# Optimization experiments

Hardware: AMD Instinct MI355X
Metric: run time of the kernel (lower is better)

The kernel has to match this reference:

```python
import jax, jax.numpy as jnp
import numpy as np

B, N, E, A, H, NT, TE = 2, 20000, 20000, 8, 256, 16, 32


def layer_norm(x, g, b, eps=1e-5):
    mu = x.mean(-1, keepdims=True)
    var = ((x - mu) ** 2).mean(-1, keepdims=True)
    return (x - mu) * jax.lax.rsqrt(var + eps) * g + b


def setup_inputs() -> dict:
    key = jax.random.key(0)
    ks = jax.random.split(key, 12)
    node_features = jax.random.normal(ks[0], (B, N, H), jnp.float32)
    hyperedge_members = jax.random.randint(ks[1], (B, E, A), 0, N)
    hyperedge_types = jax.random.randint(ks[2], (B, E), 0, NT)
    hyperedge_mask = jax.random.bernoulli(ks[3], 0.8, (B, E, A))
    edge_type_table = jax.random.normal(ks[4], (NT, TE), jnp.float32)
    W_enc = jax.random.normal(ks[5], (H + TE, H), jnp.float32) / np.sqrt(H + TE)
    b_enc = jnp.zeros((H,), jnp.float32)
    g_enc = jnp.ones((H,), jnp.float32)
    be_enc = jnp.zeros((H,), jnp.float32)
    W_upd = jax.random.normal(ks[6], (2 * H, H), jnp.float32) / np.sqrt(2 * H)
    b_upd = jnp.zeros((H,), jnp.float32)
    g_upd = jnp.ones((H,), jnp.float32)
    be_upd = jnp.zeros((H,), jnp.float32)
    return dict(node_features=node_features, hyperedge_members=hyperedge_members,
                hyperedge_types=hyperedge_types, hyperedge_mask=hyperedge_mask,
                edge_type_table=edge_type_table, W_enc=W_enc, b_enc=b_enc,
                g_enc=g_enc, be_enc=be_enc, W_upd=W_upd, b_upd=b_upd,
                g_upd=g_upd, be_upd=be_upd)


def reference(node_features, hyperedge_members, hyperedge_types, hyperedge_mask,
              edge_type_table, W_enc, b_enc, g_enc, be_enc,
              W_upd, b_upd, g_upd, be_upd):
    b, n, h = node_features.shape
    members = jnp.clip(hyperedge_members, 0, n - 1)          # [B,E,A]
    m = hyperedge_mask.astype(node_features.dtype)           # [B,E,A]

    # gather member features per hyperedge: [B,E,A,H]
    gathered = jax.vmap(lambda nf, idx: nf[idx])(node_features, members)
    gathered = gathered * m[..., None]
    cnt = jnp.clip(m.sum(-1, keepdims=True), 1.0, None)       # [B,E,1]
    pooled = gathered.sum(2) / cnt                            # [B,E,H]

    edge_emb = edge_type_table[hyperedge_types]               # [B,E,32]
    x = jnp.concatenate([pooled, edge_emb], -1) @ W_enc + b_enc
    edge_feat = layer_norm(jax.nn.gelu(x, approximate=False), g_enc, be_enc)  # [B,E,H]

    # scatter-add edge features back to member nodes (masked)
    def scat(ef, idx, mm):
        contrib = (ef[:, None, :] * mm[..., None]).reshape(-1, h)   # [E*A,H]
        flat = idx.reshape(-1)
        upd = jnp.zeros((n, h), ef.dtype).at[flat].add(contrib)
        c = jnp.zeros((n,), ef.dtype).at[flat].add(mm.reshape(-1))
        return upd, c

    upd, c = jax.vmap(scat)(edge_feat, members, m)            # [B,N,H], [B,N]
    upd = upd / jnp.clip(c, 1.0, None)[..., None]

    y = jnp.concatenate([node_features, upd], -1) @ W_upd + b_upd
    return layer_norm(jax.nn.gelu(y, approximate=False), g_upd, be_upd)
```

## Files before the change

kernel.cpp:

```cpp
#include <hip/hip_runtime.h>
#include <math.h>

#define Bq 2
#define Nn 20000
#define Ee 20000
#define Aa 8
#define Hh 256
#define TEe 32
#define NTy 16
constexpr int BE   = Bq * Ee;
constexpr int BN   = Bq * Nn;
constexpr int KTE  = 8;
constexpr int KTU  = 16;
constexpr int LDA  = 264;
constexpr int CAP  = 64;
constexpr int PB_DET = 256;
constexpr int PB_ZD  = 64;
constexpr int NINIT  = PB_DET + PB_ZD + 1;
constexpr int PB_PKE  = 32;
constexpr int PB_PKU  = 64;
constexpr int PB_TB   = 1;
constexpr int PB_FILL = 640;
constexpr int NPREP   = PB_PKE + PB_PKU + PB_TB + PB_FILL;

typedef __attribute__((ext_vector_type(8))) short bf16x8;
typedef __attribute__((ext_vector_type(4))) float f32x4;
typedef unsigned short u16;
typedef unsigned int   u32;

__device__ __forceinline__ u16 f2bf(float f) {
    u32 u = __float_as_uint(f);
    u32 r = u + 0x7FFFu + ((u >> 16) & 1u);
    return (u16)(r >> 16);
}
__device__ __forceinline__ float bf2f(u16 h) {
    return __uint_as_float(((u32)h) << 16);
}
__device__ __forceinline__ float gelu_f(float x) {
    return 0.5f * x * (1.f + erff(x * 0.70710678118654752440f));
}
__device__ __forceinline__ f32x4 mfma16(bf16x8 a, bf16x8 b, f32x4 c) {
    return __builtin_amdgcn_mfma_f32_16x16x32_bf16(a, b, c, 0, 0, 0);
}

__device__ __forceinline__ float mask_at(const void* mp, int flag, int i) {
    if (flag & 2) return ((const float*)mp)[i];
    if (flag & 1) return ((const unsigned char*)mp)[i] ? 1.f : 0.f;
    return ((const int*)mp)[i] ? 1.f : 0.f;
}

__global__ __launch_bounds__(256) void k_init(const unsigned int* __restrict__ mw,
                                              int nmw, int* __restrict__ flag,
                                              int* __restrict__ deg,
                                              float4* __restrict__ dummy) {
    const int bid = blockIdx.x;
    const int tid = threadIdx.x;
    if (bid < PB_DET) {
        int found = 0;
        for (int i = bid * 256 + tid; i < nmw; i += PB_DET * 256) {
            unsigned int w = mw[i];
            if (w == 0x3F800000u) found |= 2;
            else if (w > 1u) found |= 1;
        }
        __shared__ int sf;
        if (tid == 0) sf = 0;
        __syncthreads();
        if (found) atomicOr(&sf, found);
        __syncthreads();
        if (tid == 0 && sf) atomicOr(flag, sf);
    } else if (bid < PB_DET + PB_ZD) {
        for (int i = (bid - PB_DET) * 256 + tid; i < BN; i += PB_ZD * 256)
            deg[i] = 0;
    } else {
        if (tid < Hh * 2 / 16) {
            float4 z; z.x = 0.f; z.y = 0.f; z.z = 0.f; z.w = 0.f;
            dummy[tid] = z;
        }
    }
}

__global__ __launch_bounds__(256) void k_prep(
    const float* __restrict__ Wenc, u16* __restrict__ WeP,
    const float* __restrict__ Wupd, u16* __restrict__ WuP,
    const float* __restrict__ ett, const float* __restrict__ benc,
    float* __restrict__ tb,
    const int* __restrict__ members, const void* __restrict__ maskp,
    const int* __restrict__ flagp, int* __restrict__ deg,
    int* __restrict__ list2) {
    __shared__ float s_e[NTy * TEe];
    const int bid = blockIdx.x;
    const int tid = threadIdx.x;

    if (bid < PB_PKE) {
        int t = bid * 256 + tid;
        int lane = t & 63, tile = t >> 6;
        int kt = tile % KTE, nt = tile / KTE;
        int kbase = kt * 32 + (lane >> 4) * 8;
        int col = nt * 16 + (lane & 15);
        u16 tmp[8];
        #pragma unroll
        for (int j = 0; j < 8; j++)
            tmp[j] = f2bf(Wenc[(size_t)(kbase + j) * Hh + col]);
        *(uint4*)(WeP + (size_t)t * 8) = *(const uint4*)tmp;
    } else if (bid < PB_PKE + PB_PKU) {
        int t = (bid - PB_PKE) * 256 + tid;
        int lane = t & 63, tile = t >> 6;
        int kt = tile % KTU, nt = tile / KTU;
        int kbase = kt * 32 + (lane >> 4) * 8;
        int col = nt * 16 + (lane & 15);
        u16 tmp[8];
        #pragma unroll
        for (int j = 0; j < 8; j++)
            tmp[j] = f2bf(Wupd[(size_t)(kbase + j) * Hh + col]);
        *(uint4*)(WuP + (size_t)t * 8) = *(const uint4*)tmp;
    } else if (bid < PB_PKE + PB_PKU + PB_TB) {
        for (int i = tid; i < NTy * TEe; i += 256) s_e[i] = ett[i];
        __syncthreads();
        float b = benc[tid];
        for (int t = 0; t < NTy; t++) {
            float acc = b;
            #pragma unroll 8
            for (int k = 0; k < TEe; k++)
                acc = fmaf(s_e[t * TEe + k], Wenc[(size_t)(Hh + k) * Hh + tid], acc);
            tb[t * Hh + tid] = acc;
        }
    } else {
        int flag = flagp[0];
        int cbid = bid - (PB_PKE + PB_PKU + PB_TB);
        for (int i = cbid * 256 + tid; i < BE * Aa; i += PB_FILL * 256) {
            if (mask_at(maskp, flag, i) != 0.f) {
                int ge = i >> 3;
                int b = ge / Ee;
                int idx = min(max(members[i], 0), Nn - 1);
                int node = b * Nn + idx;
                int slot = atomicAdd(&deg[node], 1);
                if (slot < CAP) list2[(size_t)node * CAP + slot] = ge;
            }
        }
    }
}

__global__ __launch_bounds__(256) void k_dualgemm(
    const float* __restrict__ nf, const bf16x8* __restrict__ WeP,
    const bf16x8* __restrict__ WuP, uint4* __restrict__ nfWe1,
    uint4* __restrict__ nfW1) {
    __shared__ __align__(16) u16 s_a[32][LDA];
    const int tid = threadIdx.x;
    const int n0  = blockIdx.x * 32;
    const int w = tid >> 6, lane = tid & 63;
    const int l15 = lane & 15, lg = lane >> 4;

    {
        const float4* nf4 = (const float4*)nf + (size_t)n0 * 64;
        #pragma unroll
        for (int i = 0; i < 8; i++) {
            int idx = i * 256 + tid;
            int r = idx >> 6, cc = idx & 63;
            float4 v = nf4[r * 64 + cc];
            ushort4 u; u.x = f2bf(v.x); u.y = f2bf(v.y);
            u.z = f2bf(v.z); u.w = f2bf(v.w);
            *(ushort4*)&s_a[r][cc * 4] = u;
        }
    }
    __syncthreads();

    f32x4 accE[2][4], accU[2][4];
    #pragma unroll
    for (int m = 0; m < 2; m++)
        #pragma unroll
        for (int n = 0; n < 4; n++) {
            accE[m][n] = (f32x4){0.f, 0.f, 0.f, 0.f};
            accU[m][n] = (f32x4){0.f, 0.f, 0.f, 0.f};
        }

    #pragma unroll
    for (int kt = 0; kt < 8; kt++) {
        bf16x8 afr[2], bfrE[4], bfrU[4];
        #pragma unroll
        for (int n = 0; n < 4; n++) {
            bfrE[n] = WeP[((size_t)((w * 4 + n) * KTE + kt)) * 64 + lane];
            bfrU[n] = WuP[((size_t)((w * 4 + n) * KTU + kt)) * 64 + lane];
        }
        #pragma unroll
        for (int m = 0; m < 2; m++)
            afr[m] = *(const bf16x8*)&s_a[m * 16 + l15][kt * 32 + lg * 8];
        #pragma unroll
        for (int m = 0; m < 2; m++)
            #pragma unroll
            for (int n = 0; n < 4; n++) {
                accE[m][n] = mfma16(afr[m], bfrE[n], accE[m][n]);
                accU[m][n] = mfma16(afr[m], bfrU[n], accU[m][n]);
            }
    }
    __syncthreads();
    #pragma unroll
    for (int m = 0; m < 2; m++)
        #pragma unroll
        for (int j = 0; j < 4; j++) {
            int r = m * 16 + lg * 4 + j;
            #pragma unroll
            for (int n = 0; n < 4; n++)
                s_a[r][w * 64 + n * 16 + l15] = f2bf(accE[m][n][j]);
        }
    __syncthreads();
    {
        const uint4* sa4 = (const uint4*)&s_a[0][0];
        #pragma unroll
        for (int i = 0; i < 4; i++) {
            int idx = i * 256 + tid;
            int r = idx >> 5, cc = idx & 31;
            nfWe1[(size_t)(n0 + r) * 32 + cc] = sa4[r * 33 + cc];
        }
    }
    __syncthreads();
    #pragma unroll
    for (int m = 0; m < 2; m++)
        #pragma unroll
        for (int j = 0; j < 4; j++) {
            int r = m * 16 + lg * 4 + j;
            #pragma unroll
            for (int n = 0; n < 4; n++)
                s_a[r][w * 64 + n * 16 + l15] = f2bf(accU[m][n][j]);
        }
    __syncthreads();
    {
        const uint4* sa4 = (const uint4*)&s_a[0][0];
        #pragma unroll
        for (int i = 0; i < 4; i++) {
            int idx = i * 256 + tid;
            int r = idx >> 5, cc = idx & 31;
            nfW1[(size_t)(n0 + r) * 32 + cc] = sa4[r * 33 + cc];
        }
    }
}

__global__ __launch_bounds__(256) void k_edge_w2(
    const int* __restrict__ members, const void* __restrict__ maskp,
    const int* __restrict__ flagp, const int* __restrict__ types,
    const u16* __restrict__ nfWe1, const float* __restrict__ tb,
    const float* __restrict__ genc, const float* __restrict__ beenc,
    const bf16x8* __restrict__ WuP, uint4* __restrict__ efW2) {
    __shared__ __align__(16) u16 s_a[32][LDA];
    const int tid = threadIdx.x;
    const int e0  = blockIdx.x * 32;
    const int w = tid >> 6, lane = tid & 63;
    const int l15 = lane & 15, lg = lane >> 4;
    const int flag = flagp[0];
    const int c4 = lane * 4;

    {
        const int ew0 = e0 + w * 8;
        int base = ew0 * Aa + lane;
        int mem_all = members[base];
        float mv_all = mask_at(maskp, flag, base);
        int er = ew0 + (lane >> 3);
        int idxv = min(max(mem_all, 0), Nn - 1) + ((er >= Ee) ? Nn : 0);

        float4 gm = *(const float4*)(genc + c4);
        float4 bt = *(const float4*)(beenc + c4);

        for (int i = 0; i < 8; i++) {
            int e = ew0 + i;
            int idx[Aa]; float m[Aa];
            float c = 0.f;
            #pragma unroll
            for (int a = 0; a < Aa; a++) {
                idx[a] = __shfl(idxv, i * Aa + a, 64);
                m[a]   = __shfl(mv_all, i * Aa + a, 64);
                c += m[a];
            }
            const float rc = 1.f / fmaxf(c, 1.f);
            ushort4 v[Aa];
            #pragma unroll
            for (int a = 0; a < Aa; a++)
                v[a] = *(const ushort4*)(nfWe1 + (size_t)idx[a] * Hh + c4);
            float a0 = 0.f, a1 = 0.f, a2 = 0.f, a3 = 0.f;
            #pragma unroll
            for (int a = 0; a < Aa; a++) {
                a0 = fmaf(m[a], bf2f(v[a].x), a0);
                a1 = fmaf(m[a], bf2f(v[a].y), a1);
                a2 = fmaf(m[a], bf2f(v[a].z), a2);
                a3 = fmaf(m[a], bf2f(v[a].w), a3);
            }
            int t = types[e];
            float4 tbv = *(const float4*)(tb + t * Hh + c4);
            float g0 = gelu_f(fmaf(a0, rc, tbv.x));
            float g1 = gelu_f(fmaf(a1, rc, tbv.y));
            float g2 = gelu_f(fmaf(a2, rc, tbv.z));
            float g3 = gelu_f(fmaf(a3, rc, tbv.w));

            float s  = g0 + g1 + g2 + g3;
            float s2 = fmaf(g0, g0, fmaf(g1, g1, fmaf(g2, g2, g3 * g3)));
            #pragma unroll
            for (int mk = 1; mk < 64; mk <<= 1) {
                s  += __shfl_xor(s, mk, 64);
                s2 += __shfl_xor(s2, mk, 64);
            }
            float mu = s * (1.f / Hh);
            float rs = rsqrtf(s2 * (1.f / Hh) - mu * mu + 1e-5f);
            ushort4 o;
            o.x = f2bf((g0 - mu) * rs * gm.x + bt.x);
            o.y = f2bf((g1 - mu) * rs * gm.y + bt.y);
            o.z = f2bf((g2 - mu) * rs * gm.z + bt.z);
            o.w = f2bf((g3 - mu) * rs * gm.w + bt.w);
            *(ushort4*)&s_a[w * 8 + i][c4] = o;
        }
    }
    __syncthreads();

    f32x4 acc[2][4];
    #pragma unroll
    for (int m = 0; m < 2; m++)
        #pragma unroll
        for (int n = 0; n < 4; n++) acc[m][n] = (f32x4){0.f, 0.f, 0.f, 0.f};

    #pragma unroll
    for (int kt = 0; kt < 8; kt++) {
        bf16x8 bfr[4], afr[2];
        #pragma unroll
        for (int n = 0; n < 4; n++)
            bfr[n] = WuP[((size_t)((w * 4 + n) * KTU + 8 + kt)) * 64 + lane];
        #pragma unroll
        for (int m = 0; m < 2; m++)
            afr[m] = *(const bf16x8*)&s_a[m * 16 + l15][kt * 32 + lg * 8];
        #pragma unroll
        for (int m = 0; m < 2; m++)
            #pragma unroll
            for (int n = 0; n < 4; n++)
                acc[m][n] = mfma16(afr[m], bfr[n], acc[m][n]);
    }
    __syncthreads();
    #pragma unroll
    for (int m = 0; m < 2; m++)
        #pragma unroll
        for (int j = 0; j < 4; j++) {
            int r = m * 16 + lg * 4 + j;
            #pragma unroll
            for (int n = 0; n < 4; n++)
                s_a[r][w * 64 + n * 16 + l15] = f2bf(acc[m][n][j]);
        }
    __syncthreads();
    const uint4* sa4 = (const uint4*)&s_a[0][0];
    #pragma unroll
    for (int i = 0; i < 4; i++) {
        int idx = i * 256 + tid;
        int r = idx >> 5, cc = idx & 31;
        efW2[(size_t)(e0 + r) * 32 + cc] = sa4[r * 33 + cc];
    }
}

__global__ __launch_bounds__(512) void k_node_final(
    const u16* __restrict__ efW2, const u16* __restrict__ nfW1,
    const int* __restrict__ deg, const int* __restrict__ list2,
    const float* __restrict__ bupd, const float* __restrict__ gupd,
    const float* __restrict__ beupd, float* __restrict__ out) {
    const int n = (blockIdx.x * 512 + threadIdx.x) >> 6;
    const int lane = threadIdx.x & 63;
    if (n >= BN) return;
    const int d = min(deg[n], CAP);
    const size_t base = (size_t)n * CAP;
    const int c4 = lane * 4;

    float a0 = 0.f, a1 = 0.f, a2 = 0.f, a3 = 0.f;
    for (int j0 = 0; j0 < d; j0 += 8) {
        int lv = (lane < 8 && (j0 + lane) < d) ? list2[base + j0 + lane] : BE;
        ushort4 v[8];
        #pragma unroll
        for (int q = 0; q < 8; q++) {
            int ge = __shfl(lv, q, 64);
            v[q] = *(const ushort4*)(efW2 + (size_t)ge * Hh + c4);
        }
        #pragma unroll
        for (int q = 0; q < 8; q++) {
            a0 += bf2f(v[q].x); a1 += bf2f(v[q].y);
            a2 += bf2f(v[q].z); a3 += bf2f(v[q].w);
        }
    }
    const float rc = 1.f / fmaxf((float)d, 1.f);
    ushort4 w1 = *(const ushort4*)(nfW1 + (size_t)n * Hh + c4);
    float4 bb = *(const float4*)(bupd + c4);
    float g0 = gelu_f(fmaf(a0, rc, bf2f(w1.x) + bb.x));
    float g1 = gelu_f(fmaf(a1, rc, bf2f(w1.y) + bb.y));
    float g2 = gelu_f(fmaf(a2, rc, bf2f(w1.z) + bb.z));
    float g3 = gelu_f(fmaf(a3, rc, bf2f(w1.w) + bb.w));

    float s  = g0 + g1 + g2 + g3;
    float s2 = fmaf(g0, g0, fmaf(g1, g1, fmaf(g2, g2, g3 * g3)));
    #pragma unroll
    for (int mk = 1; mk < 64; mk <<= 1) {
        s  += __shfl_xor(s, mk, 64);
        s2 += __shfl_xor(s2, mk, 64);
    }
    float mu = s * (1.f / Hh);
    float rs = rsqrtf(s2 * (1.f / Hh) - mu * mu + 1e-5f);

    float4 gm = *(const float4*)(gupd + c4);
    float4 bt = *(const float4*)(beupd + c4);
    float4 o;
    o.x = (g0 - mu) * rs * gm.x + bt.x;
    o.y = (g1 - mu) * rs * gm.y + bt.y;
    o.z = (g2 - mu) * rs * gm.z + bt.z;
    o.w = (g3 - mu) * rs * gm.w + bt.w;
    *(float4*)(out + (size_t)n * Hh + c4) = o;
}

extern "C" void kernel_launch(void* const* d_in, const int* in_sizes, int n_in,
                              void* d_out, int out_size, void* d_ws, size_t ws_size,
                              hipStream_t stream) {
    const float* nf    = (const float*)d_in[0];
    const int* members = (const int*)d_in[1];
    const int* types   = (const int*)d_in[2];
    const void* maskp  = d_in[3];
    const float* ett   = (const float*)d_in[4];
    const float* Wenc  = (const float*)d_in[5];
    const float* benc  = (const float*)d_in[6];
    const float* genc  = (const float*)d_in[7];
    const float* beenc = (const float*)d_in[8];
    const float* Wupd  = (const float*)d_in[9];
    const float* bupd  = (const float*)d_in[10];
    const float* gupd  = (const float*)d_in[11];
    const float* beupd = (const float*)d_in[12];
    float* out = (float*)d_out;

    int* ip    = (int*)d_ws;
    int* flag  = ip;
    int* deg   = ip + 64;
    int* list2 = deg + BN;
    char* p    = (char*)(list2 + (size_t)BN * CAP);
    u16* efW2b  = (u16*)p;   p += (size_t)(BE + 1) * Hh * 2;
    u16* nfW1b  = (u16*)p;   p += (size_t)BN * Hh * 2;
    u16* nfWe1b = (u16*)p;   p += (size_t)BN * Hh * 2;
    u16* We1P   = (u16*)p;   p += (size_t)16 * KTE * 64 * 8 * 2;
    u16* WupdP  = (u16*)p;   p += (size_t)16 * KTU * 64 * 8 * 2;
    float* tb   = (float*)p;

    hipMemsetAsync(flag, 0, 256, stream);
    hipLaunchKernelGGL(k_init, dim3(NINIT), dim3(256), 0, stream,
                       (const unsigned int*)maskp, BE * Aa / 4, flag, deg,
                       (float4*)(efW2b + (size_t)BE * Hh));
    hipLaunchKernelGGL(k_prep, dim3(NPREP), dim3(256), 0, stream,
                       Wenc, We1P, Wupd, WupdP, ett, benc, tb,
                       members, maskp, flag, deg, list2);
    hipLaunchKernelGGL(k_dualgemm, dim3(BN / 32), dim3(256), 0, stream,
                       nf, (const bf16x8*)We1P, (const bf16x8*)WupdP,
                       (uint4*)nfWe1b, (uint4*)nfW1b);
    hipLaunchKernelGGL(k_edge_w2, dim3(BE / 32), dim3(256), 0, stream,
                       members, maskp, flag, types, nfWe1b, tb, genc, beenc,
                       (const bf16x8*)WupdP, (uint4*)efW2b);
    hipLaunchKernelGGL(k_node_final, dim3(BN * 64 / 512), dim3(512), 0, stream,
                       efW2b, nfW1b, deg, list2, bupd, gupd, beupd, out);
}
```

Baseline: 127.2 us.

## Merge init into prep, fuse list fill with dual GEMM, widen gather loads

Folds the mask-type detection and weight packing into one prep kernel, zeroes the degree array with the memset, and runs the node-list fill alongside the dual GEMM in one launch, removing a kernel launch and its serialization point. The edge and node gather loops now have each half-wave load 8 bf16 values (16 bytes) from a different member or edge, combining the halves with a cross-lane xor shuffle. This halves the number of gather iterations and widens each memory access, at the cost of extra shuffles and register use.

```diff
diff --git a/kernel.cpp b/kernel.cpp
--- a/kernel.cpp
+++ b/kernel.cpp
@@ -14,16 +14,16 @@
 constexpr int KTU  = 16;
 constexpr int LDA  = 264;
 constexpr int CAP  = 64;
-constexpr int PB_DET = 256;
-constexpr int PB_ZD  = 64;
-constexpr int NINIT  = PB_DET + PB_ZD + 1;
+constexpr int PB_DET  = 256;
 constexpr int PB_PKE  = 32;
 constexpr int PB_PKU  = 64;
 constexpr int PB_TB   = 1;
+constexpr int NPREP   = PB_DET + PB_PKE + PB_PKU + PB_TB + 1;
 constexpr int PB_FILL = 640;
-constexpr int NPREP   = PB_PKE + PB_PKU + PB_TB + PB_FILL;
+constexpr int NFD     = PB_FILL + BN / 32;
 
 typedef __attribute__((ext_vector_type(8))) short bf16x8;
+typedef __attribute__((ext_vector_type(8))) unsigned short u16x8;
 typedef __attribute__((ext_vector_type(4))) float f32x4;
 typedef unsigned short u16;
 typedef unsigned int   u32;
@@ -49,12 +49,16 @@
     return ((const int*)mp)[i] ? 1.f : 0.f;
 }
 
-__global__ __launch_bounds__(256) void k_init(const unsigned int* __restrict__ mw,
-                                              int nmw, int* __restrict__ flag,
-                                              int* __restrict__ deg,
-                                              float4* __restrict__ dummy) {
+__global__ __launch_bounds__(256) void k_prep(
+    const unsigned int* __restrict__ mw, int nmw, int* __restrict__ flag,
+    const float* __restrict__ Wenc, u16* __restrict__ WeP,
+    const float* __restrict__ Wupd, u16* __restrict__ WuP,
+    const float* __restrict__ ett, const float* __restrict__ benc,
+    float* __restrict__ tb, float4* __restrict__ dummy) {
+    __shared__ float s_e[NTy * TEe];
     const int bid = blockIdx.x;
     const int tid = threadIdx.x;
+
     if (bid < PB_DET) {
         int found = 0;
         for (int i = bid * 256 + tid; i < nmw; i += PB_DET * 256) {
@@ -68,31 +72,8 @@
         if (found) atomicOr(&sf, found);
         __syncthreads();
         if (tid == 0 && sf) atomicOr(flag, sf);
-    } else if (bid < PB_DET + PB_ZD) {
-        for (int i = (bid - PB_DET) * 256 + tid; i < BN; i += PB_ZD * 256)
-            deg[i] = 0;
-    } else {
-        if (tid < Hh * 2 / 16) {
-            float4 z; z.x = 0.f; z.y = 0.f; z.z = 0.f; z.w = 0.f;
-            dummy[tid] = z;
-        }
-    }
-}
-
-__global__ __launch_bounds__(256) void k_prep(
-    const float* __restrict__ Wenc, u16* __restrict__ WeP,
-    const float* __restrict__ Wupd, u16* __restrict__ WuP,
-    const float* __restrict__ ett, const float* __restrict__ benc,
-    float* __restrict__ tb,
-    const int* __restrict__ members, const void* __restrict__ maskp,
-    const int* __restrict__ flagp, int* __restrict__ deg,
-    int* __restrict__ list2) {
-    __shared__ float s_e[NTy * TEe];
-    const int bid = blockIdx.x;
-    const int tid = threadIdx.x;
-
-    if (bid < PB_PKE) {
-        int t = bid * 256 + tid;
+    } else if (bid < PB_DET + PB_PKE) {
+        int t = (bid - PB_DET) * 256 + tid;
         int lane = t & 63, tile = t >> 6;
         int kt = tile % KTE, nt = tile / KTE;
         int kbase = kt * 32 + (lane >> 4) * 8;
@@ -102,8 +83,8 @@
         for (int j = 0; j < 8; j++)
             tmp[j] = f2bf(Wenc[(size_t)(kbase + j) * Hh + col]);
         *(uint4*)(WeP + (size_t)t * 8) = *(const uint4*)tmp;
-    } else if (bid < PB_PKE + PB_PKU) {
-        int t = (bid - PB_PKE) * 256 + tid;
+    } else if (bid < PB_DET + PB_PKE + PB_PKU) {
+        int t = (bid - PB_DET - PB_PKE) * 256 + tid;
         int lane = t & 63, tile = t >> 6;
         int kt = tile % KTU, nt = tile / KTU;
         int kbase = kt * 32 + (lane >> 4) * 8;
@@ -113,7 +94,7 @@
         for (int j = 0; j < 8; j++)
             tmp[j] = f2bf(Wupd[(size_t)(kbase + j) * Hh + col]);
         *(uint4*)(WuP + (size_t)t * 8) = *(const uint4*)tmp;
-    } else if (bid < PB_PKE + PB_PKU + PB_TB) {
+    } else if (bid < PB_DET + PB_PKE + PB_PKU + PB_TB) {
         for (int i = tid; i < NTy * TEe; i += 256) s_e[i] = ett[i];
         __syncthreads();
         float b = benc[tid];
@@ -125,9 +106,27 @@
             tb[t * Hh + tid] = acc;
         }
     } else {
+        if (tid < Hh * 2 / 16) {
+            float4 z; z.x = 0.f; z.y = 0.f; z.z = 0.f; z.w = 0.f;
+            dummy[tid] = z;
+        }
+    }
+}
+
+__global__ __launch_bounds__(256) void k_fill_dual(
+    const int* __restrict__ members, const void* __restrict__ maskp,
+    const int* __restrict__ flagp, int* __restrict__ deg,
+    int* __restrict__ list2,
+    const float* __restrict__ nf, const bf16x8* __restrict__ WeP,
+    const bf16x8* __restrict__ WuP, uint4* __restrict__ nfWe1,
+    uint4* __restrict__ nfW1) {
+    __shared__ __align__(16) u16 s_a[32][LDA];
+    const int bid = blockIdx.x;
+    const int tid = threadIdx.x;
+
+    if (bid < PB_FILL) {
         int flag = flagp[0];
-        int cbid = bid - (PB_PKE + PB_PKU + PB_TB);
-        for (int i = cbid * 256 + tid; i < BE * Aa; i += PB_FILL * 256) {
+        for (int i = bid * 256 + tid; i < BE * Aa; i += PB_FILL * 256) {
             if (mask_at(maskp, flag, i) != 0.f) {
                 int ge = i >> 3;
                 int b = ge / Ee;
@@ -137,16 +136,9 @@
                 if (slot < CAP) list2[(size_t)node * CAP + slot] = ge;
             }
         }
-    }
-}
-
-__global__ __launch_bounds__(256) void k_dualgemm(
-    const float* __restrict__ nf, const bf16x8* __restrict__ WeP,
-    const bf16x8* __restrict__ WuP, uint4* __restrict__ nfWe1,
-    uint4* __restrict__ nfW1) {
-    __shared__ __align__(16) u16 s_a[32][LDA];
-    const int tid = threadIdx.x;
-    const int n0  = blockIdx.x * 32;
+        return;
+    }
+    const int n0 = (bid - PB_FILL) * 32;
     const int w = tid >> 6, lane = tid & 63;
     const int l15 = lane & 15, lg = lane >> 4;
 
@@ -246,7 +238,9 @@
     const int w = tid >> 6, lane = tid & 63;
     const int l15 = lane & 15, lg = lane >> 4;
     const int flag = flagp[0];
-    const int c4 = lane * 4;
+    const int colb = (lane & 31) * 8;
+    const int half = lane >> 5;
+    const int colw = colb + half * 4;
 
     {
         const int ew0 = e0 + w * 8;
@@ -256,39 +250,43 @@
         int er = ew0 + (lane >> 3);
         int idxv = min(max(mem_all, 0), Nn - 1) + ((er >= Ee) ? Nn : 0);
 
-        float4 gm = *(const float4*)(genc + c4);
-        float4 bt = *(const float4*)(beenc + c4);
+        float4 gm = *(const float4*)(genc + colw);
+        float4 bt = *(const float4*)(beenc + colw);
 
         for (int i = 0; i < 8; i++) {
             int e = ew0 + i;
-            int idx[Aa]; float m[Aa];
             float c = 0.f;
             #pragma unroll
-            for (int a = 0; a < Aa; a++) {
-                idx[a] = __shfl(idxv, i * Aa + a, 64);
-                m[a]   = __shfl(mv_all, i * Aa + a, 64);
-                c += m[a];
+            for (int a = 0; a < Aa; a++) c += __shfl(mv_all, i * 8 + a, 64);
+            u16x8 v[4]; float mw_[4];
+            #pragma unroll
+            for (int q = 0; q < 4; q++) {
+                int a = 2 * q + half;
+                int gi = __shfl(idxv, i * 8 + a, 64);
+                mw_[q] = __shfl(mv_all, i * 8 + a, 64);
+                v[q] = *(const u16x8*)(nfWe1 + (size_t)gi * Hh + colb);
             }
+            float acc[8];
+            #pragma unroll
+            for (int k = 0; k < 8; k++) acc[k] = 0.f;
+            #pragma unroll
+            for (int q = 0; q < 4; q++)
+                #pragma unroll
+                for (int k = 0; k < 8; k++)
+                    acc[k] = fmaf(mw_[q], bf2f(v[q][k]), acc[k]);
+            #pragma unroll
+            for (int k = 0; k < 8; k++) acc[k] += __shfl_xor(acc[k], 32, 64);
             const float rc = 1.f / fmaxf(c, 1.f);
-            ushort4 v[Aa];
-            #pragma unroll
-            for (int a = 0; a < Aa; a++)
-                v[a] = *(const ushort4*)(nfWe1 + (size_t)idx[a] * Hh + c4);
-            float a0 = 0.f, a1 = 0.f, a2 = 0.f, a3 = 0.f;
-            #pragma unroll
-            for (int a = 0; a < Aa; a++) {
-                a0 = fmaf(m[a], bf2f(v[a].x), a0);
-                a1 = fmaf(m[a], bf2f(v[a].y), a1);
-                a2 = fmaf(m[a], bf2f(v[a].z), a2);
-                a3 = fmaf(m[a], bf2f(v[a].w), a3);
-            }
+            float x0 = half ? acc[4] : acc[0];
+            float x1 = half ? acc[5] : acc[1];
+            float x2 = half ? acc[6] : acc[2];
+            float x3 = half ? acc[7] : acc[3];
             int t = types[e];
-            float4 tbv = *(const float4*)(tb + t * Hh + c4);
-            float g0 = gelu_f(fmaf(a0, rc, tbv.x));
-            float g1 = gelu_f(fmaf(a1, rc, tbv.y));
-            float g2 = gelu_f(fmaf(a2, rc, tbv.z));
-            float g3 = gelu_f(fmaf(a3, rc, tbv.w));
-
+            float4 tbv = *(const float4*)(tb + t * Hh + colw);
+            float g0 = gelu_f(fmaf(x0, rc, tbv.x));
+            float g1 = gelu_f(fmaf(x1, rc, tbv.y));
+            float g2 = gelu_f(fmaf(x2, rc, tbv.z));
+            float g3 = gelu_f(fmaf(x3, rc, tbv.w));
             float s  = g0 + g1 + g2 + g3;
             float s2 = fmaf(g0, g0, fmaf(g1, g1, fmaf(g2, g2, g3 * g3)));
             #pragma unroll
@@ -303,7 +301,7 @@
             o.y = f2bf((g1 - mu) * rs * gm.y + bt.y);
             o.z = f2bf((g2 - mu) * rs * gm.z + bt.z);
             o.w = f2bf((g3 - mu) * rs * gm.w + bt.w);
-            *(ushort4*)&s_a[w * 8 + i][c4] = o;
+            *(ushort4*)&s_a[w * 8 + i][colw] = o;
         }
     }
     __syncthreads();
@@ -359,30 +357,45 @@
     if (n >= BN) return;
     const int d = min(deg[n], CAP);
     const size_t base = (size_t)n * CAP;
-    const int c4 = lane * 4;
-
-    float a0 = 0.f, a1 = 0.f, a2 = 0.f, a3 = 0.f;
+    const int colb = (lane & 31) * 8;
+    const int half = lane >> 5;
+    const int colw = colb + half * 4;
+
+    int lv = (lane < d) ? list2[base + lane] : BE;
+
+    float acc[8];
+    #pragma unroll
+    for (int k = 0; k < 8; k++) acc[k] = 0.f;
+
     for (int j0 = 0; j0 < d; j0 += 8) {
-        int lv = (lane < 8 && (j0 + lane) < d) ? list2[base + j0 + lane] : BE;
-        ushort4 v[8];
-        #pragma unroll
-        for (int q = 0; q < 8; q++) {
-            int ge = __shfl(lv, q, 64);
-            v[q] = *(const ushort4*)(efW2 + (size_t)ge * Hh + c4);
-        }
-        #pragma unroll
-        for (int q = 0; q < 8; q++) {
-            a0 += bf2f(v[q].x); a1 += bf2f(v[q].y);
-            a2 += bf2f(v[q].z); a3 += bf2f(v[q].w);
-        }
-    }
+        u16x8 v[4];
+        #pragma unroll
+        for (int q = 0; q < 4; q++) {
+            int jj = j0 + 2 * q + half;
+            int ge = __shfl(lv, jj & 63, 64);
+            if (jj >= d) ge = BE;
+            v[q] = *(const u16x8*)(efW2 + (size_t)ge * Hh + colb);
+        }
+        #pragma unroll
+        for (int q = 0; q < 4; q++)
+            #pragma unroll
+            for (int k = 0; k < 8; k++)
+                acc[k] += bf2f(v[q][k]);
+    }
+    #pragma unroll
+    for (int k = 0; k < 8; k++) acc[k] += __shfl_xor(acc[k], 32, 64);
+
     const float rc = 1.f / fmaxf((float)d, 1.f);
-    ushort4 w1 = *(const ushort4*)(nfW1 + (size_t)n * Hh + c4);
-    float4 bb = *(const float4*)(bupd + c4);
-    float g0 = gelu_f(fmaf(a0, rc, bf2f(w1.x) + bb.x));
-    float g1 = gelu_f(fmaf(a1, rc, bf2f(w1.y) + bb.y));
-    float g2 = gelu_f(fmaf(a2, rc, bf2f(w1.z) + bb.z));
-    float g3 = gelu_f(fmaf(a3, rc, bf2f(w1.w) + bb.w));
+    float x0 = half ? acc[4] : acc[0];
+    float x1 = half ? acc[5] : acc[1];
+    float x2 = half ? acc[6] : acc[2];
+    float x3 = half ? acc[7] : acc[3];
+    ushort4 w1 = *(const ushort4*)(nfW1 + (size_t)n * Hh + colw);
+    float4 bb = *(const float4*)(bupd + colw);
+    float g0 = gelu_f(fmaf(x0, rc, bf2f(w1.x) + bb.x));
+    float g1 = gelu_f(fmaf(x1, rc, bf2f(w1.y) + bb.y));
+    float g2 = gelu_f(fmaf(x2, rc, bf2f(w1.z) + bb.z));
+    float g3 = gelu_f(fmaf(x3, rc, bf2f(w1.w) + bb.w));
 
     float s  = g0 + g1 + g2 + g3;
     float s2 = fmaf(g0, g0, fmaf(g1, g1, fmaf(g2, g2, g3 * g3)));
@@ -394,14 +407,14 @@
     float mu = s * (1.f / Hh);
     float rs = rsqrtf(s2 * (1.f / Hh) - mu * mu + 1e-5f);
 
-    float4 gm = *(const float4*)(gupd + c4);
-    float4 bt = *(const float4*)(beupd + c4);
+    float4 gm = *(const float4*)(gupd + colw);
+    float4 bt = *(const float4*)(beupd + colw);
     float4 o;
     o.x = (g0 - mu) * rs * gm.x + bt.x;
     o.y = (g1 - mu) * rs * gm.y + bt.y;
     o.z = (g2 - mu) * rs * gm.z + bt.z;
     o.w = (g3 - mu) * rs * gm.w + bt.w;
-    *(float4*)(out + (size_t)n * Hh + c4) = o;
+    *(float4*)(out + (size_t)n * Hh + colw) = o;
 }
 
 extern "C" void kernel_launch(void* const* d_in, const int* in_sizes, int n_in,
@@ -434,14 +447,13 @@
     u16* WupdP  = (u16*)p;   p += (size_t)16 * KTU * 64 * 8 * 2;
     float* tb   = (float*)p;
 
-    hipMemsetAsync(flag, 0, 256, stream);
-    hipLaunchKernelGGL(k_init, dim3(NINIT), dim3(256), 0, stream,
-                       (const unsigned int*)maskp, BE * Aa / 4, flag, deg,
+    hipMemsetAsync(ip, 0, (size_t)(64 + BN) * 4, stream);
+    hipLaunchKernelGGL(k_prep, dim3(NPREP), dim3(256), 0, stream,
+                       (const unsigned int*)maskp, BE * Aa / 4, flag,
+                       Wenc, We1P, Wupd, WupdP, ett, benc, tb,
                        (float4*)(efW2b + (size_t)BE * Hh));
-    hipLaunchKernelGGL(k_prep, dim3(NPREP), dim3(256), 0, stream,
-                       Wenc, We1P, Wupd, WupdP, ett, benc, tb,
-                       members, maskp, flag, deg, list2);
-    hipLaunchKernelGGL(k_dualgemm, dim3(BN / 32), dim3(256), 0, stream,
+    hipLaunchKernelGGL(k_fill_dual, dim3(NFD), dim3(256), 0, stream,
+                       members, maskp, flag, deg, list2,
                        nf, (const bf16x8*)We1P, (const bf16x8*)WupdP,
                        (uint4*)nfWe1b, (uint4*)nfW1b);
     hipLaunchKernelGGL(k_edge_w2, dim3(BE / 32), dim3(256), 0, stream,
```

Result: faster. 123.7 us (-2.7%).
